# Optimization experiments

Hardware: AMD Instinct MI355X
Metric: run time of the kernel (lower is better)

## Reference

```python
import jax, jax.numpy as jnp
import numpy as np


def _haar_dwt2(x):
    # x: [b, H, W] -> (ll, lh, hl, hh), each [b, H/2, W/2]; orthonormal 2D Haar
    a = x[:, ::2, ::2]
    b = x[:, ::2, 1::2]
    c = x[:, 1::2, ::2]
    d = x[:, 1::2, 1::2]
    ll = (a + b + c + d) * 0.5
    lh = (a + b - c - d) * 0.5  # detail along rows (frames)
    hl = (a - b + c - d) * 0.5  # detail along cols (features)
    hh = (a - b - c + d) * 0.5
    return ll, lh, hl, hh


def _haar_idwt2(ll, lh, hl, hh):
    a = (ll + lh + hl + hh) * 0.5
    b = (ll + lh - hl - hh) * 0.5
    c = (ll - lh + hl - hh) * 0.5
    d = (ll - lh - hl + hh) * 0.5
    B, H2, W2 = ll.shape
    out = jnp.zeros((B, 2 * H2, 2 * W2), ll.dtype)
    out = out.at[:, ::2, ::2].set(a)
    out = out.at[:, ::2, 1::2].set(b)
    out = out.at[:, 1::2, ::2].set(c)
    out = out.at[:, 1::2, 1::2].set(d)
    return out


def _interp_linear_last(x, m):
    # linear interpolation along last dim from linspace(0,1,n) to linspace(0,1,m)
    n = x.shape[-1]
    pos = jnp.linspace(0.0, 1.0, m, dtype=x.dtype) * (n - 1)
    i0 = jnp.clip(jnp.floor(pos).astype(jnp.int32), 0, n - 2)
    w = pos - i0.astype(x.dtype)
    return x[..., i0] * (1.0 - w) + x[..., i0 + 1] * w


def setup_inputs() -> dict:
    key = jax.random.key(0)
    k0, k1, k2 = jax.random.split(key, 3)
    b, f, c, hidden = 128, 256, 512, 2048
    x = jax.random.normal(k0, (b, f, c), dtype=jnp.float32)
    fc1_w = jax.random.normal(k1, (hidden, c), dtype=jnp.float32) * 0.02
    fc1_b = jnp.zeros((hidden,), dtype=jnp.float32)
    fc2_w = jax.random.normal(k2, (c // 2, hidden), dtype=jnp.float32) * 0.02
    fc2_b = jnp.zeros((c // 2,), dtype=jnp.float32)
    return {"x": x, "fc1_w": fc1_w, "fc1_b": fc1_b, "fc2_w": fc2_w, "fc2_b": fc2_b}


def reference(x, fc1_w, fc1_b, fc2_w, fc2_b):
    b, f, c = x.shape
    ll, lh, hl, hh = _haar_dwt2(x)               # [b, f/2, c/2] each
    ll_up = _interp_linear_last(ll, c)           # [b, f/2, c]
    h = jax.nn.gelu(jnp.einsum('bfc,hc->bfh', ll_up, fc1_w) + fc1_b, approximate=False)
    ll_new = jnp.einsum('bfh,oh->bfo', h, fc2_w) + fc2_b  # [b, f/2, c/2]
    return _haar_idwt2(ll_new, lh, hl, hh)       # [b, f, c]
```

## Files before the change

kernel.cpp:

```cpp
#include <hip/hip_runtime.h>
#include <hip/hip_bf16.h>
#include <stdint.h>

typedef __bf16 bf16;
typedef __attribute__((ext_vector_type(8)))  __bf16 bf16x8;
typedef __attribute__((ext_vector_type(16))) float  f32x16;

#define B_DIM 128
#define F_DIM 256
#define C_DIM 512
#define HID   2048
#define C2    256
#define MROWS 16384

static constexpr size_t OFF_W1 = 0;
static constexpr size_t OFF_W2 = 1u << 20;

__device__ __forceinline__ unsigned short bfbits(float f) {
    bf16 h = (bf16)f;
    return __builtin_bit_cast(unsigned short, h);
}

__global__ __launch_bounds__(256) void prep_kernel(
    const float* __restrict__ w1, const float* __restrict__ w2,
    bf16* __restrict__ w1pp, bf16* __restrict__ w2pp)
{
    const int blk = blockIdx.x;
    const int t = threadIdx.x;
    if (blk < 2048) {
        int idx = blk * 256 + t;
        int h = idx >> 8, k = idx & 255;
        const float* wrow = w1 + (size_t)h * C_DIM;
        float acc = 0.f;
        int jlo = (k == 0) ? 0 : (int)((float)(k - 1) * (511.0f / 255.0f));
        int jhi = (int)((float)(k + 1) * (511.0f / 255.0f)) + 1;
        if (jhi > 511) jhi = 511;
        for (int j = jlo; j <= jhi; ++j) {
            float pos = (float)j * (255.0f / 511.0f);
            int i0 = (int)pos;
            if (i0 > 254) i0 = 254;
            float w = pos - (float)i0;
            float coef = (i0 == k) ? (1.0f - w) : ((i0 + 1 == k) ? w : 0.0f);
            acc += coef * wrow[j];
        }
        size_t frag = (size_t)(h >> 5) * 16 + (k >> 4);
        size_t lane = (size_t)(((k >> 3) & 1) << 5 | (h & 31));
        w1pp[frag * 512 + lane * 8 + (k & 7)] = (bf16)acc;
    } else {
        int idx2 = (blk - 2048) * 256 + t;
        int c2 = idx2 >> 11, hid = idx2 & 2047;
        float v = w2[(size_t)c2 * HID + hid];
        size_t frag = (size_t)(c2 >> 5) * 128 + (hid >> 4);
        size_t lane = (size_t)(((hid >> 3) & 1) << 5 | (c2 & 31));
        w2pp[frag * 512 + lane * 8 + (hid & 7)] = (bf16)v;
    }
}

__global__ __launch_bounds__(512, 2) void fused_mlp(
    const bf16* __restrict__ w1pp, const bf16* __restrict__ w2pp,
    const float* __restrict__ b1, const float* __restrict__ b2,
    const float* __restrict__ x, float* __restrict__ out)
{
    __shared__ __align__(16) char smem[65536];
    char* hsm = smem + 32768;

    const int tid = threadIdx.x;
    const int l   = tid & 63;
    const int wv  = tid >> 6;
    const int R0  = blockIdx.x * 64;
    const char* w1B = (const char*)w1pp;
    const char* w2B = (const char*)w2pp;

    {
        const int r  = tid >> 3;
        const int rg = r >> 5;
        const int gbf = R0 + r;
        const float* xr0 = x + ((size_t)(gbf >> 7) * F_DIM + (size_t)(gbf & 127) * 2) * C_DIM;
        const float* xr1 = xr0 + C_DIM;
#pragma unroll
        for (int jj = 0; jj < 4; ++jj) {
            int j = (tid & 7) * 4 + jj;
            float4 a[4], b[4];
#pragma unroll
            for (int i = 0; i < 4; ++i) {
                a[i] = ((const float4*)xr0)[j * 4 + i];
                b[i] = ((const float4*)xr1)[j * 4 + i];
            }
            const float* pa = (const float*)a;
            const float* pb = (const float*)b;
            bf16x8 pk;
#pragma unroll
            for (int e = 0; e < 8; ++e)
                pk[e] = (bf16)(0.5f * (pa[2*e] + pa[2*e+1] + pb[2*e] + pb[2*e+1]));
            int kf   = j >> 1;
            int lane = ((j & 1) << 5) | (r & 31);
            *(bf16x8*)(smem + (((kf * 2 + rg) * 64) + lane) * 16) = pk;
        }
    }
    __syncthreads();

    f32x16 acc2_0{}, acc2_1{};

    auto geluwrite = [&](const f32x16& A, int nf, int rg, int hc) {
        const float bs = b1[hc * 512 + wv * 64 + nf * 32 + (l & 31)];
#pragma unroll
        for (int reg = 0; reg < 16; ++reg) {
            float v = A[reg] + bs;
            float tt = v * (0.79788456080f + 0.03567740814f * v * v);
            float g = v / (1.0f + __expf(-2.0f * tt));
            float gp = __builtin_bit_cast(float,
                __builtin_amdgcn_mov_dpp(__builtin_bit_cast(int, g), 0xB1, 0xF, 0xF, true));
            if (!(l & 1)) {
                unsigned u = (unsigned)bfbits(g) | ((unsigned)bfbits(gp) << 16);
                int crow  = (reg & 3) + 8 * (reg >> 2) + 4 * (l >> 5);
                int kf2   = (wv & 3) * 4 + nf * 2 + ((l & 31) >> 4);
                int lane2 = ((l >> 3) & 1) << 5 | crow;
                *(unsigned*)(hsm + ((kf2 * 2 + rg) * 64 + lane2) * 16 + (l & 7) * 2) = u;
            }
        }
    };

    auto g2half = [&](int hc, int hs) {
        bf16x8 wr2[4];
        const char* w2f = w2B + ((size_t)(wv * 128 + hc * 32 + hs * 16)) * 1024 + (size_t)l * 16;
#pragma unroll
        for (int i = 0; i < 4; ++i) wr2[i] = *(const bf16x8*)(w2f + i * 1024);
#pragma unroll
        for (int ks = 0; ks < 16; ++ks) {
            bf16x8 h0 = *(const bf16x8*)(hsm + ((ks * 2 + 0) * 64 + l) * 16);
            bf16x8 h1 = *(const bf16x8*)(hsm + ((ks * 2 + 1) * 64 + l) * 16);
            acc2_0 = __builtin_amdgcn_mfma_f32_32x32x16_bf16(h0, wr2[ks & 3], acc2_0, 0, 0, 0);
            acc2_1 = __builtin_amdgcn_mfma_f32_32x32x16_bf16(h1, wr2[ks & 3], acc2_1, 0, 0, 0);
            if (ks + 4 < 16)
                wr2[ks & 3] = *(const bf16x8*)(w2f + (ks + 4) * 1024);
        }
    };

#pragma unroll 1
    for (int hc = 0; hc < 4; ++hc) {
        f32x16 a1_00{}, a1_01{}, a1_10{}, a1_11{};
        bf16x8 wr0[4], wr1[4];
        const char* w1f0 = w1B + ((size_t)((hc * 16 + wv * 2 + 0) * 16)) * 1024 + (size_t)l * 16;
        const char* w1f1 = w1B + ((size_t)((hc * 16 + wv * 2 + 1) * 16)) * 1024 + (size_t)l * 16;
#pragma unroll
        for (int i = 0; i < 4; ++i) {
            wr0[i] = *(const bf16x8*)(w1f0 + i * 1024);
            wr1[i] = *(const bf16x8*)(w1f1 + i * 1024);
        }
#pragma unroll
        for (int ks = 0; ks < 16; ++ks) {
            bf16x8 a0 = *(const bf16x8*)(smem + ((ks * 2 + 0) * 64 + l) * 16);
            bf16x8 a1 = *(const bf16x8*)(smem + ((ks * 2 + 1) * 64 + l) * 16);
            a1_00 = __builtin_amdgcn_mfma_f32_32x32x16_bf16(a0, wr0[ks & 3], a1_00, 0, 0, 0);
            a1_01 = __builtin_amdgcn_mfma_f32_32x32x16_bf16(a1, wr0[ks & 3], a1_01, 0, 0, 0);
            a1_10 = __builtin_amdgcn_mfma_f32_32x32x16_bf16(a0, wr1[ks & 3], a1_10, 0, 0, 0);
            a1_11 = __builtin_amdgcn_mfma_f32_32x32x16_bf16(a1, wr1[ks & 3], a1_11, 0, 0, 0);
            if (ks + 4 < 16) {
                wr0[ks & 3] = *(const bf16x8*)(w1f0 + (ks + 4) * 1024);
                wr1[ks & 3] = *(const bf16x8*)(w1f1 + (ks + 4) * 1024);
            }
        }

        if (wv < 4) {
            geluwrite(a1_00, 0, 0, hc); geluwrite(a1_01, 0, 1, hc);
            geluwrite(a1_10, 1, 0, hc); geluwrite(a1_11, 1, 1, hc);
        }
        __syncthreads();
        g2half(hc, 0);
        __syncthreads();
        if (wv >= 4) {
            geluwrite(a1_00, 0, 0, hc); geluwrite(a1_01, 0, 1, hc);
            geluwrite(a1_10, 1, 0, hc); geluwrite(a1_11, 1, 1, hc);
        }
        __syncthreads();
        g2half(hc, 1);
        __syncthreads();
    }

    {
        const int c2 = wv * 32 + (l & 31);
        const float bs = b2[c2];
#pragma unroll
        for (int rg = 0; rg < 2; ++rg) {
            const f32x16& A = rg ? acc2_1 : acc2_0;
#pragma unroll
            for (int reg = 0; reg < 16; ++reg) {
                int R = R0 + rg * 32 + (reg & 3) + 8 * (reg >> 2) + 4 * (l >> 5);
                int b = R >> 7, f2 = R & 127;
                const float* xr = x + ((size_t)b * F_DIM + (size_t)f2 * 2) * C_DIM;
                float2 p0 = ((const float2*)xr)[c2];
                float2 p1 = ((const float2*)(xr + C_DIM))[c2];
                float llo = 0.5f * (p0.x + p0.y + p1.x + p1.y);
                float d = 0.5f * ((A[reg] + bs) - llo);
                float2 o0, o1;
                o0.x = p0.x + d; o0.y = p0.y + d;
                o1.x = p1.x + d; o1.y = p1.y + d;
                float* orow = out + ((size_t)b * F_DIM + (size_t)f2 * 2) * C_DIM;
                ((float2*)orow)[c2] = o0;
                ((float2*)(orow + C_DIM))[c2] = o1;
            }
        }
    }
}

extern "C" void kernel_launch(void* const* d_in, const int* in_sizes, int n_in,
                              void* d_out, int out_size, void* d_ws, size_t ws_size,
                              hipStream_t stream) {
    const float* x     = (const float*)d_in[0];
    const float* fc1_w = (const float*)d_in[1];
    const float* fc1_b = (const float*)d_in[2];
    const float* fc2_w = (const float*)d_in[3];
    const float* fc2_b = (const float*)d_in[4];
    float* out = (float*)d_out;

    char* ws = (char*)d_ws;
    bf16* w1pp = (bf16*)(ws + OFF_W1);
    bf16* w2pp = (bf16*)(ws + OFF_W2);

    prep_kernel<<<4096, 256, 0, stream>>>(fc1_w, fc2_w, w1pp, w2pp);
    fused_mlp<<<MROWS / 64, 512, 0, stream>>>(w1pp, w2pp, fc1_b, fc2_b, x, out);
}
```

Measured before the change: 108.8 us.

## Halve row tile to 32, keep LL fragments in registers, batch weight loads

The fused MLP block now handles 32 rows instead of 64, which doubles the grid to 512 blocks and cuts shared memory to 48KB. The 16 input LL fragments are loaded once into registers. Each hidden chunk of 512 is then computed in one pass followed by a single sync, replacing the previous split across two half-waves. Weight fragments are loaded in batches of 8 and separated from the MFMAs by sched_barrier. The trade-off is that each block re-reads the full weights for only half as many rows, doubling weight traffic per output row, in exchange for more parallelism and fewer barriers.

```diff
diff --git a/kernel.cpp b/kernel.cpp
--- a/kernel.cpp
+++ b/kernel.cpp
@@ -20,6 +20,7 @@
     bf16 h = (bf16)f;
     return __builtin_bit_cast(unsigned short, h);
 }
+#define SCHED0() __builtin_amdgcn_sched_barrier(0)
 
 __global__ __launch_bounds__(256) void prep_kernel(
     const float* __restrict__ w1, const float* __restrict__ w2,
@@ -61,25 +62,27 @@
     const float* __restrict__ b1, const float* __restrict__ b2,
     const float* __restrict__ x, float* __restrict__ out)
 {
-    __shared__ __align__(16) char smem[65536];
-    char* hsm = smem + 32768;
+    __shared__ __align__(16) char smem[49152];
+    char* hsm = smem + 16384;
 
     const int tid = threadIdx.x;
     const int l   = tid & 63;
     const int wv  = tid >> 6;
-    const int R0  = blockIdx.x * 64;
+    const int sub = wv >> 2;
+    const int sl4 = wv & 3;
+    const int R0  = blockIdx.x * 32;
     const char* w1B = (const char*)w1pp;
     const char* w2B = (const char*)w2pp;
 
     {
-        const int r  = tid >> 3;
-        const int rg = r >> 5;
+        const int r = tid & 31;
+        const int s = tid >> 5;
         const int gbf = R0 + r;
         const float* xr0 = x + ((size_t)(gbf >> 7) * F_DIM + (size_t)(gbf & 127) * 2) * C_DIM;
         const float* xr1 = xr0 + C_DIM;
 #pragma unroll
-        for (int jj = 0; jj < 4; ++jj) {
-            int j = (tid & 7) * 4 + jj;
+        for (int jj = 0; jj < 2; ++jj) {
+            int j = s * 2 + jj;
             float4 a[4], b[4];
 #pragma unroll
             for (int i = 0; i < 4; ++i) {
@@ -92,88 +95,76 @@
 #pragma unroll
             for (int e = 0; e < 8; ++e)
                 pk[e] = (bf16)(0.5f * (pa[2*e] + pa[2*e+1] + pb[2*e] + pb[2*e+1]));
-            int kf   = j >> 1;
-            int lane = ((j & 1) << 5) | (r & 31);
-            *(bf16x8*)(smem + (((kf * 2 + rg) * 64) + lane) * 16) = pk;
+            *(bf16x8*)(smem + s * 1024 + (size_t)((jj << 5) | r) * 16) = pk;
         }
     }
     __syncthreads();
 
-    f32x16 acc2_0{}, acc2_1{};
-
-    auto geluwrite = [&](const f32x16& A, int nf, int rg, int hc) {
-        const float bs = b1[hc * 512 + wv * 64 + nf * 32 + (l & 31)];
-#pragma unroll
-        for (int reg = 0; reg < 16; ++reg) {
-            float v = A[reg] + bs;
-            float tt = v * (0.79788456080f + 0.03567740814f * v * v);
-            float g = v / (1.0f + __expf(-2.0f * tt));
-            float gp = __builtin_bit_cast(float,
-                __builtin_amdgcn_mov_dpp(__builtin_bit_cast(int, g), 0xB1, 0xF, 0xF, true));
-            if (!(l & 1)) {
-                unsigned u = (unsigned)bfbits(g) | ((unsigned)bfbits(gp) << 16);
-                int crow  = (reg & 3) + 8 * (reg >> 2) + 4 * (l >> 5);
-                int kf2   = (wv & 3) * 4 + nf * 2 + ((l & 31) >> 4);
-                int lane2 = ((l >> 3) & 1) << 5 | crow;
-                *(unsigned*)(hsm + ((kf2 * 2 + rg) * 64 + lane2) * 16 + (l & 7) * 2) = u;
-            }
-        }
-    };
-
-    auto g2half = [&](int hc, int hs) {
-        bf16x8 wr2[4];
-        const char* w2f = w2B + ((size_t)(wv * 128 + hc * 32 + hs * 16)) * 1024 + (size_t)l * 16;
-#pragma unroll
-        for (int i = 0; i < 4; ++i) wr2[i] = *(const bf16x8*)(w2f + i * 1024);
-#pragma unroll
-        for (int ks = 0; ks < 16; ++ks) {
-            bf16x8 h0 = *(const bf16x8*)(hsm + ((ks * 2 + 0) * 64 + l) * 16);
-            bf16x8 h1 = *(const bf16x8*)(hsm + ((ks * 2 + 1) * 64 + l) * 16);
-            acc2_0 = __builtin_amdgcn_mfma_f32_32x32x16_bf16(h0, wr2[ks & 3], acc2_0, 0, 0, 0);
-            acc2_1 = __builtin_amdgcn_mfma_f32_32x32x16_bf16(h1, wr2[ks & 3], acc2_1, 0, 0, 0);
-            if (ks + 4 < 16)
-                wr2[ks & 3] = *(const bf16x8*)(w2f + (ks + 4) * 1024);
-        }
-    };
+    bf16x8 llr[16];
+#pragma unroll
+    for (int kf = 0; kf < 16; ++kf)
+        llr[kf] = *(const bf16x8*)(smem + kf * 1024 + (size_t)l * 16);
+
+    f32x16 acc2{};
 
 #pragma unroll 1
-    for (int hc = 0; hc < 4; ++hc) {
-        f32x16 a1_00{}, a1_01{}, a1_10{}, a1_11{};
-        bf16x8 wr0[4], wr1[4];
-        const char* w1f0 = w1B + ((size_t)((hc * 16 + wv * 2 + 0) * 16)) * 1024 + (size_t)l * 16;
-        const char* w1f1 = w1B + ((size_t)((hc * 16 + wv * 2 + 1) * 16)) * 1024 + (size_t)l * 16;
-#pragma unroll
-        for (int i = 0; i < 4; ++i) {
-            wr0[i] = *(const bf16x8*)(w1f0 + i * 1024);
-            wr1[i] = *(const bf16x8*)(w1f1 + i * 1024);
-        }
-#pragma unroll
-        for (int ks = 0; ks < 16; ++ks) {
-            bf16x8 a0 = *(const bf16x8*)(smem + ((ks * 2 + 0) * 64 + l) * 16);
-            bf16x8 a1 = *(const bf16x8*)(smem + ((ks * 2 + 1) * 64 + l) * 16);
-            a1_00 = __builtin_amdgcn_mfma_f32_32x32x16_bf16(a0, wr0[ks & 3], a1_00, 0, 0, 0);
-            a1_01 = __builtin_amdgcn_mfma_f32_32x32x16_bf16(a1, wr0[ks & 3], a1_01, 0, 0, 0);
-            a1_10 = __builtin_amdgcn_mfma_f32_32x32x16_bf16(a0, wr1[ks & 3], a1_10, 0, 0, 0);
-            a1_11 = __builtin_amdgcn_mfma_f32_32x32x16_bf16(a1, wr1[ks & 3], a1_11, 0, 0, 0);
-            if (ks + 4 < 16) {
-                wr0[ks & 3] = *(const bf16x8*)(w1f0 + (ks + 4) * 1024);
-                wr1[ks & 3] = *(const bf16x8*)(w1f1 + (ks + 4) * 1024);
-            }
-        }
-
-        if (wv < 4) {
-            geluwrite(a1_00, 0, 0, hc); geluwrite(a1_01, 0, 1, hc);
-            geluwrite(a1_10, 1, 0, hc); geluwrite(a1_11, 1, 1, hc);
+    for (int pc = 0; pc < 4; ++pc) {
+        f32x16 acc1_0{}, acc1_1{};
+        const int hb = pc * 16 + sub * 8 + sl4 * 2;
+        const char* w1f = w1B + ((size_t)hb * 16) * 1024 + (size_t)l * 16;
+#pragma unroll
+        for (int g = 0; g < 2; ++g) {
+            bf16x8 wf0[8], wf1[8];
+#pragma unroll
+            for (int i = 0; i < 8; ++i) {
+                wf0[i] = *(const bf16x8*)(w1f + (g * 8 + i) * 1024);
+                wf1[i] = *(const bf16x8*)(w1f + (16 + g * 8 + i) * 1024);
+            }
+            SCHED0();
+#pragma unroll
+            for (int i = 0; i < 8; ++i) {
+                acc1_0 = __builtin_amdgcn_mfma_f32_32x32x16_bf16(llr[g * 8 + i], wf0[i], acc1_0, 0, 0, 0);
+                acc1_1 = __builtin_amdgcn_mfma_f32_32x32x16_bf16(llr[g * 8 + i], wf1[i], acc1_1, 0, 0, 0);
+            }
+        }
+
+#pragma unroll
+        for (int nf = 0; nf < 2; ++nf) {
+            const f32x16& A = nf ? acc1_1 : acc1_0;
+            const int cin = sub * 256 + sl4 * 64 + nf * 32 + (l & 31);
+            const float bs = b1[pc * 512 + cin];
+            const int kf2 = cin >> 4;
+#pragma unroll
+            for (int reg = 0; reg < 16; ++reg) {
+                float v = A[reg] + bs;
+                float tt = v * (0.79788456080f + 0.03567740814f * v * v);
+                float g = v / (1.0f + __expf(-2.0f * tt));
+                float gp = __builtin_bit_cast(float,
+                    __builtin_amdgcn_mov_dpp(__builtin_bit_cast(int, g), 0xB1, 0xF, 0xF, true));
+                if (!(l & 1)) {
+                    unsigned u = (unsigned)bfbits(g) | ((unsigned)bfbits(gp) << 16);
+                    int crow = (reg & 3) + 8 * (reg >> 2) + 4 * (l >> 5);
+                    int lane2 = (((l >> 3) & 1) << 5) | crow;
+                    *(unsigned*)(hsm + kf2 * 1024 + lane2 * 16 + (l & 7) * 2) = u;
+                }
+            }
         }
         __syncthreads();
-        g2half(hc, 0);
-        __syncthreads();
-        if (wv >= 4) {
-            geluwrite(a1_00, 0, 0, hc); geluwrite(a1_01, 0, 1, hc);
-            geluwrite(a1_10, 1, 0, hc); geluwrite(a1_11, 1, 1, hc);
-        }
-        __syncthreads();
-        g2half(hc, 1);
+
+        const char* w2f = w2B + ((size_t)(wv * 128 + pc * 32)) * 1024 + (size_t)l * 16;
+#pragma unroll
+        for (int g = 0; g < 4; ++g) {
+            bf16x8 wf[8];
+#pragma unroll
+            for (int i = 0; i < 8; ++i)
+                wf[i] = *(const bf16x8*)(w2f + (g * 8 + i) * 1024);
+            SCHED0();
+#pragma unroll
+            for (int i = 0; i < 8; ++i) {
+                bf16x8 hfr = *(const bf16x8*)(hsm + (g * 8 + i) * 1024 + (size_t)l * 16);
+                acc2 = __builtin_amdgcn_mfma_f32_32x32x16_bf16(hfr, wf[i], acc2, 0, 0, 0);
+            }
+        }
         __syncthreads();
     }
 
@@ -181,24 +172,20 @@
         const int c2 = wv * 32 + (l & 31);
         const float bs = b2[c2];
 #pragma unroll
-        for (int rg = 0; rg < 2; ++rg) {
-            const f32x16& A = rg ? acc2_1 : acc2_0;
-#pragma unroll
-            for (int reg = 0; reg < 16; ++reg) {
-                int R = R0 + rg * 32 + (reg & 3) + 8 * (reg >> 2) + 4 * (l >> 5);
-                int b = R >> 7, f2 = R & 127;
-                const float* xr = x + ((size_t)b * F_DIM + (size_t)f2 * 2) * C_DIM;
-                float2 p0 = ((const float2*)xr)[c2];
-                float2 p1 = ((const float2*)(xr + C_DIM))[c2];
-                float llo = 0.5f * (p0.x + p0.y + p1.x + p1.y);
-                float d = 0.5f * ((A[reg] + bs) - llo);
-                float2 o0, o1;
-                o0.x = p0.x + d; o0.y = p0.y + d;
-                o1.x = p1.x + d; o1.y = p1.y + d;
-                float* orow = out + ((size_t)b * F_DIM + (size_t)f2 * 2) * C_DIM;
-                ((float2*)orow)[c2] = o0;
-                ((float2*)(orow + C_DIM))[c2] = o1;
-            }
+        for (int reg = 0; reg < 16; ++reg) {
+            int R = R0 + (reg & 3) + 8 * (reg >> 2) + 4 * (l >> 5);
+            int b = R >> 7, f2 = R & 127;
+            const float* xr = x + ((size_t)b * F_DIM + (size_t)f2 * 2) * C_DIM;
+            float2 p0 = ((const float2*)xr)[c2];
+            float2 p1 = ((const float2*)(xr + C_DIM))[c2];
+            float llo = 0.5f * (p0.x + p0.y + p1.x + p1.y);
+            float d = 0.5f * ((acc2[reg] + bs) - llo);
+            float2 o0, o1;
+            o0.x = p0.x + d; o0.y = p0.y + d;
+            o1.x = p1.x + d; o1.y = p1.y + d;
+            float* orow = out + ((size_t)b * F_DIM + (size_t)f2 * 2) * C_DIM;
+            ((float2*)orow)[c2] = o0;
+            ((float2*)(orow + C_DIM))[c2] = o1;
         }
     }
 }
@@ -218,5 +205,5 @@
     bf16* w2pp = (bf16*)(ws + OFF_W2);
 
     prep_kernel<<<4096, 256, 0, stream>>>(fc1_w, fc2_w, w1pp, w2pp);
-    fused_mlp<<<MROWS / 64, 512, 0, stream>>>(w1pp, w2pp, fc1_b, fc2_b, x, out);
-}
+    fused_mlp<<<MROWS / 32, 512, 0, stream>>>(w1pp, w2pp, fc1_b, fc2_b, x, out);
+}
```

After: 100.8 us. 1.08x faster.
